# Kernel optimization log

Measured on AMD Instinct MI355X. Metric: run time of the kernel, lower is better.

Reference implementation:

```python
import jax, jax.numpy as jnp
import numpy as np
import math

B, S, D, H = 2, 2048, 1024, 16
HD = D // H  # head_dims = 64


def setup_inputs() -> dict:
    key = jax.random.key(0)
    ks = jax.random.split(key, 8)
    sc = 1.0 / math.sqrt(D)
    return {
        "queries": jax.random.normal(ks[0], (B, S, D), jnp.float32),
        "keys":    jax.random.normal(ks[1], (B, S, D), jnp.float32),
        "values":  jax.random.normal(ks[2], (B, S, D), jnp.float32),
        # causal mask: 1 where attending allowed, 0 where blocked (masked_fill on ==0)
        "mask": jnp.tril(jnp.ones((S, S), jnp.int32)),
        "Wq": jax.random.normal(ks[3], (D, D), jnp.float32) * sc,
        "bq": jnp.zeros((D,), jnp.float32),
        "Wk": jax.random.normal(ks[4], (D, D), jnp.float32) * sc,
        "bk": jnp.zeros((D,), jnp.float32),
        "Wv": jax.random.normal(ks[5], (D, D), jnp.float32) * sc,
        "bv": jnp.zeros((D,), jnp.float32),
        "Wo": jax.random.normal(ks[6], (D, D), jnp.float32) * sc,
        "bo": jnp.zeros((D,), jnp.float32),
    }


def _split_heads(x):
    # (B, S, D) -> (B, H, S, HD)
    return x.reshape(B, S, H, HD).transpose(0, 2, 1, 3)


def reference(queries, keys, values, mask, Wq, bq, Wk, bk, Wv, bv, Wo, bo):
    q = queries @ Wq + bq
    k = keys @ Wk + bk
    # NOTE: faithful to source quirk — V is projected from the ALREADY-PROJECTED keys
    # (original: keys = self.W_keys(keys); values = self.W_values(keys))
    v = k @ Wv + bv
    q, k, v = _split_heads(q), _split_heads(k), _split_heads(v)
    # naive full NxN attention, as in the source
    scores = jnp.einsum("bhqd,bhkd->bhqk", q, k) / math.sqrt(HD)
    scores = jnp.where(mask == 0, jnp.float32(-1e9), scores)
    probs = jax.nn.softmax(scores, axis=-1)
    attn = jnp.einsum("bhqk,bhkd->bhqd", probs, v)
    attn = attn.transpose(0, 2, 1, 3).reshape(B, S, D)
    return attn @ Wo + bo
```

## Files before the change

### kernel.cpp

```cpp
#include <hip/hip_runtime.h>

typedef unsigned short u16;
typedef unsigned int u32;
typedef __bf16 bf16x8 __attribute__((ext_vector_type(8)));
typedef float f32x4 __attribute__((ext_vector_type(4)));
typedef float f32x16 __attribute__((ext_vector_type(16)));
typedef unsigned int u32x4v __attribute__((ext_vector_type(4)));

#define MFMA16(a, b, c) __builtin_amdgcn_mfma_f32_16x16x32_bf16(a, b, c, 0, 0, 0)
#define MFMA32(a, b, c) __builtin_amdgcn_mfma_f32_32x32x16_bf16(a, b, c, 0, 0, 0)

__device__ __forceinline__ void gload16(const void* g, void* l) {
  __builtin_amdgcn_global_load_lds((const __attribute__((address_space(1))) void*)g,
                                   (__attribute__((address_space(3))) void*)l, 16, 0, 0);
}

__device__ __forceinline__ u16 f2bf(float f) {
  u32 u = __builtin_bit_cast(u32, f);
  u += 0x7fffu + ((u >> 16) & 1u);
  return (u16)(u >> 16);
}
__device__ __forceinline__ u32 pack2(float a, float b) {
  u32 r;
  asm("v_cvt_pk_bf16_f32 %0, %1, %2" : "=v"(r) : "v"(a), "v"(b));
  return r;
}

__global__ __launch_bounds__(256) void prep_kernel(
    const float* __restrict__ q, const float* __restrict__ k,
    u16* __restrict__ qb, u16* __restrict__ kb,
    const float* W0, const float* W1, const float* W2, const float* W3,
    u16* T0, u16* T1, u16* T2, u16* T3) {
  __shared__ float tile[64][65];
  const int z = blockIdx.z;
  if (z < 2) {
    const float* src = z ? k : q;
    u16* dst = z ? kb : qb;
    const int bid = blockIdx.y * 16 + blockIdx.x;
    const size_t base = (size_t)bid * 256 + threadIdx.x;
#pragma unroll
    for (int i = 0; i < 16; i++) {
      size_t idx = base + (size_t)i * 65536;
      float4 v = ((const float4*)src)[idx];
      uint2 o;
      o.x = pack2(v.x, v.y);
      o.y = pack2(v.z, v.w);
      ((uint2*)dst)[idx] = o;
    }
    return;
  }
  const float* W = z == 2 ? W0 : z == 3 ? W1 : z == 4 ? W2 : W3;
  u16* T = z == 2 ? T0 : z == 3 ? T1 : z == 4 ? T2 : T3;
  int tr = blockIdx.y * 64, tc = blockIdx.x * 64;
  int tid = threadIdx.x;
  int c4 = (tid & 15) * 4, r0 = tid >> 4;
#pragma unroll
  for (int i = 0; i < 4; i++) {
    int r = r0 + i * 16;
    float4 v = *(const float4*)(W + (size_t)(tr + r) * 1024 + tc + c4);
    tile[r][c4 + 0] = v.x; tile[r][c4 + 1] = v.y;
    tile[r][c4 + 2] = v.z; tile[r][c4 + 3] = v.w;
  }
  __syncthreads();
#pragma unroll
  for (int i = 0; i < 2; i++) {
    int c = tid + i * 256;
    int n = c >> 3, kg = c & 7;
    uint4 o;
    o.x = pack2(tile[kg * 8 + 0][n], tile[kg * 8 + 1][n]);
    o.y = pack2(tile[kg * 8 + 2][n], tile[kg * 8 + 3][n]);
    o.z = pack2(tile[kg * 8 + 4][n], tile[kg * 8 + 5][n]);
    o.w = pack2(tile[kg * 8 + 6][n], tile[kg * 8 + 7][n]);
    *(uint4*)(T + (size_t)(tc + n) * 1024 + tr + kg * 8) = o;
  }
}

template <int MODE>
__global__ __launch_bounds__(256) void gemm_kernel(
    const u16* A0, const u16* B0, const float* bias0, void* C0, float scale0,
    const u16* A1, const u16* B1, const float* bias1, void* C1, float scale1,
    int M, int N, int K) {
  const u16* A = A0; const u16* Bt = B0; const float* bias = bias0; void* Cout = C0;
  float scale = scale0;
  if (blockIdx.z) { A = A1; Bt = B1; bias = bias1; Cout = C1; scale = scale1; }

  __shared__ __attribute__((aligned(16))) char sAB[49152];
  const int tid = threadIdx.x, lane = tid & 63, w = tid >> 6;
  const int l15 = lane & 15, quad = lane >> 4;
  const int wm = (w >> 1) * 64, wn = (w & 1) * 32;
  const int m0 = blockIdx.y * 128, n0 = blockIdx.x * 64;

  const int lrow = lane >> 3, lcg = (lane & 7) ^ lrow;
  const u16* aP[4]; const u16* bP[2];
#pragma unroll
  for (int i = 0; i < 4; i++)
    aP[i] = A + (size_t)(m0 + w * 32 + i * 8 + lrow) * K + lcg * 8;
#pragma unroll
  for (int i = 0; i < 2; i++)
    bP[i] = Bt + (size_t)(n0 + w * 16 + i * 8 + lrow) * K + lcg * 8;

  int aoff[4], boff[2];
#pragma unroll
  for (int t = 0; t < 4; t++) {
    int ra = wm + t * 16 + l15;
    aoff[t] = ra * 128 + ((quad ^ (ra & 7)) * 16);
  }
#pragma unroll
  for (int t = 0; t < 2; t++) {
    int rb = wn + t * 16 + l15;
    boff[t] = 16384 + rb * 128 + ((quad ^ (rb & 7)) * 16);
  }

#pragma unroll
  for (int i = 0; i < 4; i++) { gload16(aP[i], sAB + w * 4096 + i * 1024); aP[i] += 64; }
#pragma unroll
  for (int i = 0; i < 2; i++) { gload16(bP[i], sAB + 16384 + w * 2048 + i * 1024); bP[i] += 64; }

  f32x4 acc[4][2] = {};
  int cur = 0;
  for (int k = 0; k < K; k += 64) {
    __syncthreads();
    if (k + 64 < K) {
      char* dst = sAB + (cur ^ 1) * 24576;
#pragma unroll
      for (int i = 0; i < 4; i++) { gload16(aP[i], dst + w * 4096 + i * 1024); aP[i] += 64; }
#pragma unroll
      for (int i = 0; i < 2; i++) { gload16(bP[i], dst + 16384 + w * 2048 + i * 1024); bP[i] += 64; }
    }
    const char* buf = sAB + cur * 24576;
#pragma unroll
    for (int kt = 0; kt < 2; kt++) {
      bf16x8 af[4], bfr[2];
#pragma unroll
      for (int t = 0; t < 4; t++) af[t] = *(const bf16x8*)(buf + (aoff[t] ^ (kt * 64)));
#pragma unroll
      for (int t = 0; t < 2; t++) bfr[t] = *(const bf16x8*)(buf + (boff[t] ^ (kt * 64)));
#pragma unroll
      for (int mt = 0; mt < 4; mt++)
#pragma unroll
        for (int nt = 0; nt < 2; nt++)
          acc[mt][nt] = MFMA16(af[mt], bfr[nt], acc[mt][nt]);
    }
    cur ^= 1;
  }

#pragma unroll
  for (int nt = 0; nt < 2; nt++) {
    int col = n0 + wn + nt * 16 + l15;
    float bv = bias[col];
#pragma unroll
    for (int mt = 0; mt < 4; mt++) {
      int row = m0 + wm + mt * 16 + quad * 4;
      if (MODE == 0) {
        u16* C = (u16*)Cout;
#pragma unroll
        for (int r = 0; r < 4; r++)
          C[(size_t)(row + r) * N + col] = f2bf((acc[mt][nt][r] + bv) * scale);
      } else if (MODE == 1) {
        u16* C = (u16*)Cout;
        int hh = col >> 6, hd = col & 63;
        int bb = row >> 11, s = row & 2047;
        uint2 o;
        o.x = pack2((acc[mt][nt][0] + bv) * scale, (acc[mt][nt][1] + bv) * scale);
        o.y = pack2((acc[mt][nt][2] + bv) * scale, (acc[mt][nt][3] + bv) * scale);
        *(uint2*)(C + ((size_t)((bb * 16 + hh) * 64 + hd) * 2048 + s)) = o;
      } else {
        float* C = (float*)Cout;
#pragma unroll
        for (int r = 0; r < 4; r++)
          C[(size_t)(row + r) * N + col] = (acc[mt][nt][r] + bv) * scale;
      }
    }
  }
}

__global__ __launch_bounds__(256, 2) void attn_kernel(const u16* __restrict__ qw,
                                                      const u16* __restrict__ kw,
                                                      const u16* __restrict__ vw,
                                                      u16* __restrict__ aout) {
  __shared__ __attribute__((aligned(16))) char sKV[4][16384];
  __shared__ float slq[4][64];
  char* sflat = (char*)sKV;
  const int bh = blockIdx.x, p = blockIdx.y;
  const int b = bh >> 4, h = bh & 15;
  const int tid = threadIdx.x, lane = tid & 63, w = tid >> 6;
  const int g = w & 1, kh = w >> 1;
  const int c = lane & 31, hi = lane >> 5;
  const int lrow = lane >> 3, lcg = (lane & 7) ^ lrow;
  const u16* kb0 = kw + (size_t)(b * 2048) * 1024 + h * 64;
  const u16* vb0 = vw + (size_t)bh * 64 * 2048;

  int koffK[4], koffV[2][2];
  {
    int krow = kh * 32 + c;
#pragma unroll
    for (int kt = 0; kt < 4; kt++)
      koffK[kt] = krow * 128 + (((kt * 2 + hi) ^ (krow & 7)) * 16);
#pragma unroll
    for (int m = 0; m < 2; m++) {
      int vrow = m * 32 + c;
#pragma unroll
      for (int kt2 = 0; kt2 < 2; kt2++)
        koffV[m][kt2] = 8192 + vrow * 128 + ((((kh * 2 + kt2) * 2 + hi) ^ (vrow & 7)) * 16);
    }
  }

  auto stage = [&](int j, int slot) {
    char* dst = sKV[slot];
#pragma unroll
    for (int i = 0; i < 2; i++) {
      int rr = w * 16 + i * 8 + lrow;
      gload16(kb0 + (size_t)(j * 64 + rr) * 1024 + lcg * 8, dst + w * 2048 + i * 1024);
      gload16(vb0 + (size_t)rr * 2048 + j * 64 + lcg * 8, dst + 8192 + w * 2048 + i * 1024);
    }
  };

  for (int phase = 0; phase < 2; ++phase) {
    const int t = phase ? (31 - p) : p;
    __syncthreads();

    bf16x8 qf[2][4];
#pragma unroll
    for (int qb2 = 0; qb2 < 2; qb2++) {
      const u16* qbase =
          qw + (size_t)(b * 2048 + t * 64 + qb2 * 32 + c) * 1024 + h * 64 + hi * 8;
#pragma unroll
      for (int kt = 0; kt < 4; kt++) qf[qb2][kt] = *(const bf16x8*)(qbase + kt * 16);
    }
    stage(0, 0);
    if (t >= 1) stage(1, 1);

    f32x16 o00 = {}, o01 = {}, o10 = {}, o11 = {};
    float ls0 = 0.f, ls1 = 0.f;
    const int R = (t + 2) >> 1;
    for (int r = 0; r < R; ++r) {
      __syncthreads();
      if (2 * r + 2 <= t) stage(2 * r + 2, (2 * r + 2) & 3);
      if (2 * r + 3 <= t) stage(2 * r + 3, (2 * r + 3) & 3);
      const int jg = 2 * r + g;
      if (jg <= t) {
        const char* buf = sKV[jg & 3];
        f32x16 S0 = {}, S1 = {};
        __builtin_amdgcn_s_setprio(1);
#pragma unroll
        for (int kt = 0; kt < 4; kt++) {
          bf16x8 kf = *(const bf16x8*)(buf + koffK[kt]);
          S0 = MFMA32(kf, qf[0][kt], S0);
          S1 = MFMA32(kf, qf[1][kt], S1);
        }
        __builtin_amdgcn_s_setprio(0);
        const bool diag = (jg == t);
        u32 pw0[8], pw1[8];
        auto epack = [&](const f32x16& S, int qc, u32* pw, float& ls) {
          float e[16];
#pragma unroll
          for (int rg = 0; rg < 16; rg++) {
            float ev = __builtin_amdgcn_exp2f(S[rg]);
            if (diag) {
              int row = kh * 32 + (rg & 3) + 8 * (rg >> 2) + 4 * hi;
              if (row > qc) ev = 0.f;
            }
            e[rg] = ev;
          }
          float sAcc = 0.f;
#pragma unroll
          for (int rg = 0; rg < 16; rg += 4)
            sAcc += (e[rg] + e[rg + 1]) + (e[rg + 2] + e[rg + 3]);
          ls += sAcc;
#pragma unroll
          for (int i = 0; i < 8; i++) pw[i] = pack2(e[2 * i], e[2 * i + 1]);
        };
        epack(S0, c, pw0, ls0);
        epack(S1, 32 + c, pw1, ls1);
        __builtin_amdgcn_s_setprio(1);
#pragma unroll
        for (int kt2 = 0; kt2 < 2; kt2++) {
          const int bb = kt2 * 4;
          auto a0 = __builtin_amdgcn_permlane32_swap(pw0[bb + 0], pw0[bb + 2], false, false);
          auto a1 = __builtin_amdgcn_permlane32_swap(pw0[bb + 1], pw0[bb + 3], false, false);
          u32x4v pq0 = {a0[0], a1[0], a0[1], a1[1]};
          bf16x8 pf0 = __builtin_bit_cast(bf16x8, pq0);
          auto b0 = __builtin_amdgcn_permlane32_swap(pw1[bb + 0], pw1[bb + 2], false, false);
          auto b1 = __builtin_amdgcn_permlane32_swap(pw1[bb + 1], pw1[bb + 3], false, false);
          u32x4v pq1 = {b0[0], b1[0], b0[1], b1[1]};
          bf16x8 pf1 = __builtin_bit_cast(bf16x8, pq1);
          bf16x8 v0 = *(const bf16x8*)(buf + koffV[0][kt2]);
          bf16x8 v1 = *(const bf16x8*)(buf + koffV[1][kt2]);
          o00 = MFMA32(v0, pf0, o00);
          o10 = MFMA32(v1, pf0, o10);
          o01 = MFMA32(v0, pf1, o01);
          o11 = MFMA32(v1, pf1, o11);
        }
        __builtin_amdgcn_s_setprio(0);
      }
    }

    ls0 += __shfl_xor(ls0, 32, 64);
    ls1 += __shfl_xor(ls1, 32, 64);
    __syncthreads();
    {
      char* myr = sflat + w * 16384;
      auto putq = [&](int qid, const f32x16& v) {
#pragma unroll
        for (int ch = 0; ch < 4; ch++) {
          f32x4 x = {v[ch * 4 + 0], v[ch * 4 + 1], v[ch * 4 + 2], v[ch * 4 + 3]};
          *(f32x4*)(myr + (qid * 4 + ch) * 1024 + lane * 16) = x;
        }
      };
      putq(0, o00); putq(1, o01); putq(2, o10); putq(3, o11);
      slq[w][hi * 32 + c] = hi ? ls1 : ls0;
    }
    __syncthreads();
    {
      f32x16 acc = {};
#pragma unroll
      for (int wv = 0; wv < 4; wv++)
#pragma unroll
        for (int ch = 0; ch < 4; ch++) {
          f32x4 rr = *(const f32x4*)(sflat + wv * 16384 + (w * 4 + ch) * 1024 + lane * 16);
          acc[ch * 4 + 0] += rr[0]; acc[ch * 4 + 1] += rr[1];
          acc[ch * 4 + 2] += rr[2]; acc[ch * 4 + 3] += rr[3];
        }
      const int q = (w & 1) * 32 + c;
      float lt = ((slq[0][q] + slq[1][q]) + (slq[2][q] + slq[3][q]));
      float inv = 1.0f / lt;
      int token = b * 2048 + t * 64 + q;
      u16* outp = aout + (size_t)token * 1024 + h * 64 + (w >> 1) * 32;
#pragma unroll
      for (int i = 0; i < 4; i++) {
        uint2 ov;
        ov.x = pack2(acc[4 * i + 0] * inv, acc[4 * i + 1] * inv);
        ov.y = pack2(acc[4 * i + 2] * inv, acc[4 * i + 3] * inv);
        *(uint2*)(outp + i * 8 + hi * 4) = ov;
      }
    }
  }
}

extern "C" void kernel_launch(void* const* d_in, const int* in_sizes, int n_in,
                              void* d_out, int out_size, void* d_ws, size_t ws_size,
                              hipStream_t stream) {
  const float* queries = (const float*)d_in[0];
  const float* keys    = (const float*)d_in[1];
  const float* Wq = (const float*)d_in[4];
  const float* bq = (const float*)d_in[5];
  const float* Wk = (const float*)d_in[6];
  const float* bk = (const float*)d_in[7];
  const float* Wv = (const float*)d_in[8];
  const float* bv = (const float*)d_in[9];
  const float* Wo = (const float*)d_in[10];
  const float* bo = (const float*)d_in[11];

  char* ws = (char*)d_ws;
  u16* qb  = (u16*)(ws);
  u16* kb  = (u16*)(ws + (8u << 20));
  u16* qP  = (u16*)(ws + (16u << 20));
  u16* kP  = (u16*)(ws);
  u16* vP  = (u16*)(ws + (8u << 20));
  u16* WqT = (u16*)(ws + (24u << 20));
  u16* WkT = (u16*)(ws + (26u << 20));
  u16* WvT = (u16*)(ws + (28u << 20));
  u16* WoT = (u16*)(ws + (30u << 20));

  const float kscale = 1.4426950408889634f / 8.0f;

  prep_kernel<<<dim3(16, 16, 6), 256, 0, stream>>>(
      queries, keys, qb, kb, Wq, Wk, Wv, Wo, WqT, WkT, WvT, WoT);
  gemm_kernel<0><<<dim3(16, 32, 2), 256, 0, stream>>>(
      qb, WqT, bq, qP, kscale, kb, WkT, bk, kP, 1.0f, 4096, 1024, 1024);
  gemm_kernel<1><<<dim3(16, 32, 1), 256, 0, stream>>>(
      kP, WvT, bv, vP, 1.0f, kP, WvT, bv, vP, 1.0f, 4096, 1024, 1024);
  attn_kernel<<<dim3(32, 16), 256, 0, stream>>>(qP, kP, vP, qP);
  gemm_kernel<2><<<dim3(16, 32, 1), 256, 0, stream>>>(
      qP, WoT, bo, d_out, 1.0f, qP, WoT, bo, d_out, 1.0f, 4096, 1024, 1024);
}
```

Baseline: 213.5 us.

## Run both causal query tiles concurrently in one 512-thread attention block

```diff
diff --git a/kernel.cpp b/kernel.cpp
--- a/kernel.cpp
+++ b/kernel.cpp
@@ -174,7 +174,7 @@
   }
 }
 
-__global__ __launch_bounds__(256, 2) void attn_kernel(const u16* __restrict__ qw,
+__global__ __launch_bounds__(512, 4) void attn_kernel(const u16* __restrict__ qw,
                                                       const u16* __restrict__ kw,
                                                       const u16* __restrict__ vw,
                                                       u16* __restrict__ aout) {
@@ -184,7 +184,10 @@
   const int bh = blockIdx.x, p = blockIdx.y;
   const int b = bh >> 4, h = bh & 15;
   const int tid = threadIdx.x, lane = tid & 63, w = tid >> 6;
-  const int g = w & 1, kh = w >> 1;
+  const int quad = w >> 2, w4 = w & 3;
+  const int g = w & 1, kh = (w >> 1) & 1;
+  const int t = quad ? (31 - p) : p;
+  const int tlong = 31 - p;
   const int c = lane & 31, hi = lane >> 5;
   const int lrow = lane >> 3, lcg = (lane & 7) ^ lrow;
   const u16* kb0 = kw + (size_t)(b * 2048) * 1024 + h * 64;
@@ -207,99 +210,94 @@
 
   auto stage = [&](int j, int slot) {
     char* dst = sKV[slot];
-#pragma unroll
-    for (int i = 0; i < 2; i++) {
-      int rr = w * 16 + i * 8 + lrow;
-      gload16(kb0 + (size_t)(j * 64 + rr) * 1024 + lcg * 8, dst + w * 2048 + i * 1024);
-      gload16(vb0 + (size_t)rr * 2048 + j * 64 + lcg * 8, dst + 8192 + w * 2048 + i * 1024);
-    }
+    int rr = w * 8 + lrow;
+    gload16(kb0 + (size_t)(j * 64 + rr) * 1024 + lcg * 8, dst + w * 1024);
+    gload16(vb0 + (size_t)rr * 2048 + j * 64 + lcg * 8, dst + 8192 + w * 1024);
   };
 
-  for (int phase = 0; phase < 2; ++phase) {
-    const int t = phase ? (31 - p) : p;
+  bf16x8 qf[2][4];
+#pragma unroll
+  for (int qb2 = 0; qb2 < 2; qb2++) {
+    const u16* qbase =
+        qw + (size_t)(b * 2048 + t * 64 + qb2 * 32 + c) * 1024 + h * 64 + hi * 8;
+#pragma unroll
+    for (int kt = 0; kt < 4; kt++) qf[qb2][kt] = *(const bf16x8*)(qbase + kt * 16);
+  }
+  stage(0, 0);
+  stage(1, 1);
+
+  f32x16 o00 = {}, o01 = {}, o10 = {}, o11 = {};
+  float ls0 = 0.f, ls1 = 0.f;
+  const int R = (tlong + 2) >> 1;
+  for (int r = 0; r < R; ++r) {
     __syncthreads();
-
-    bf16x8 qf[2][4];
-#pragma unroll
-    for (int qb2 = 0; qb2 < 2; qb2++) {
-      const u16* qbase =
-          qw + (size_t)(b * 2048 + t * 64 + qb2 * 32 + c) * 1024 + h * 64 + hi * 8;
-#pragma unroll
-      for (int kt = 0; kt < 4; kt++) qf[qb2][kt] = *(const bf16x8*)(qbase + kt * 16);
-    }
-    stage(0, 0);
-    if (t >= 1) stage(1, 1);
-
-    f32x16 o00 = {}, o01 = {}, o10 = {}, o11 = {};
-    float ls0 = 0.f, ls1 = 0.f;
-    const int R = (t + 2) >> 1;
-    for (int r = 0; r < R; ++r) {
-      __syncthreads();
-      if (2 * r + 2 <= t) stage(2 * r + 2, (2 * r + 2) & 3);
-      if (2 * r + 3 <= t) stage(2 * r + 3, (2 * r + 3) & 3);
-      const int jg = 2 * r + g;
-      if (jg <= t) {
-        const char* buf = sKV[jg & 3];
-        f32x16 S0 = {}, S1 = {};
-        __builtin_amdgcn_s_setprio(1);
-#pragma unroll
-        for (int kt = 0; kt < 4; kt++) {
-          bf16x8 kf = *(const bf16x8*)(buf + koffK[kt]);
-          S0 = MFMA32(kf, qf[0][kt], S0);
-          S1 = MFMA32(kf, qf[1][kt], S1);
+    if (2 * r + 2 <= tlong) stage(2 * r + 2, (2 * r + 2) & 3);
+    if (2 * r + 3 <= tlong) stage(2 * r + 3, (2 * r + 3) & 3);
+    const int jg = 2 * r + g;
+    if (jg <= t) {
+      const char* buf = sKV[jg & 3];
+      f32x16 S0 = {}, S1 = {};
+      __builtin_amdgcn_s_setprio(1);
+#pragma unroll
+      for (int kt = 0; kt < 4; kt++) {
+        bf16x8 kf = *(const bf16x8*)(buf + koffK[kt]);
+        S0 = MFMA32(kf, qf[0][kt], S0);
+        S1 = MFMA32(kf, qf[1][kt], S1);
+      }
+      __builtin_amdgcn_s_setprio(0);
+      const bool diag = (jg == t);
+      u32 pw0[8], pw1[8];
+      auto epack = [&](const f32x16& S, int qc, u32* pw, float& ls) {
+        float e[16];
+#pragma unroll
+        for (int rg = 0; rg < 16; rg++) {
+          float ev = __builtin_amdgcn_exp2f(S[rg]);
+          if (diag) {
+            int row = kh * 32 + (rg & 3) + 8 * (rg >> 2) + 4 * hi;
+            if (row > qc) ev = 0.f;
+          }
+          e[rg] = ev;
         }
-        __builtin_amdgcn_s_setprio(0);
-        const bool diag = (jg == t);
-        u32 pw0[8], pw1[8];
-        auto epack = [&](const f32x16& S, int qc, u32* pw, float& ls) {
-          float e[16];
-#pragma unroll
-          for (int rg = 0; rg < 16; rg++) {
-            float ev = __builtin_amdgcn_exp2f(S[rg]);
-            if (diag) {
-              int row = kh * 32 + (rg & 3) + 8 * (rg >> 2) + 4 * hi;
-              if (row > qc) ev = 0.f;
-            }
-            e[rg] = ev;
-          }
-          float sAcc = 0.f;
-#pragma unroll
-          for (int rg = 0; rg < 16; rg += 4)
-            sAcc += (e[rg] + e[rg + 1]) + (e[rg + 2] + e[rg + 3]);
-          ls += sAcc;
-#pragma unroll
-          for (int i = 0; i < 8; i++) pw[i] = pack2(e[2 * i], e[2 * i + 1]);
-        };
-        epack(S0, c, pw0, ls0);
-        epack(S1, 32 + c, pw1, ls1);
-        __builtin_amdgcn_s_setprio(1);
-#pragma unroll
-        for (int kt2 = 0; kt2 < 2; kt2++) {
-          const int bb = kt2 * 4;
-          auto a0 = __builtin_amdgcn_permlane32_swap(pw0[bb + 0], pw0[bb + 2], false, false);
-          auto a1 = __builtin_amdgcn_permlane32_swap(pw0[bb + 1], pw0[bb + 3], false, false);
-          u32x4v pq0 = {a0[0], a1[0], a0[1], a1[1]};
-          bf16x8 pf0 = __builtin_bit_cast(bf16x8, pq0);
-          auto b0 = __builtin_amdgcn_permlane32_swap(pw1[bb + 0], pw1[bb + 2], false, false);
-          auto b1 = __builtin_amdgcn_permlane32_swap(pw1[bb + 1], pw1[bb + 3], false, false);
-          u32x4v pq1 = {b0[0], b1[0], b0[1], b1[1]};
-          bf16x8 pf1 = __builtin_bit_cast(bf16x8, pq1);
-          bf16x8 v0 = *(const bf16x8*)(buf + koffV[0][kt2]);
-          bf16x8 v1 = *(const bf16x8*)(buf + koffV[1][kt2]);
-          o00 = MFMA32(v0, pf0, o00);
-          o10 = MFMA32(v1, pf0, o10);
-          o01 = MFMA32(v0, pf1, o01);
-          o11 = MFMA32(v1, pf1, o11);
-        }
-        __builtin_amdgcn_s_setprio(0);
+        float sAcc = 0.f;
+#pragma unroll
+        for (int rg = 0; rg < 16; rg += 4)
+          sAcc += (e[rg] + e[rg + 1]) + (e[rg + 2] + e[rg + 3]);
+        ls += sAcc;
+#pragma unroll
+        for (int i = 0; i < 8; i++) pw[i] = pack2(e[2 * i], e[2 * i + 1]);
+      };
+      epack(S0, c, pw0, ls0);
+      epack(S1, 32 + c, pw1, ls1);
+      __builtin_amdgcn_s_setprio(1);
+#pragma unroll
+      for (int kt2 = 0; kt2 < 2; kt2++) {
+        const int bb = kt2 * 4;
+        auto a0 = __builtin_amdgcn_permlane32_swap(pw0[bb + 0], pw0[bb + 2], false, false);
+        auto a1 = __builtin_amdgcn_permlane32_swap(pw0[bb + 1], pw0[bb + 3], false, false);
+        u32x4v pq0 = {a0[0], a1[0], a0[1], a1[1]};
+        bf16x8 pf0 = __builtin_bit_cast(bf16x8, pq0);
+        auto b0 = __builtin_amdgcn_permlane32_swap(pw1[bb + 0], pw1[bb + 2], false, false);
+        auto b1 = __builtin_amdgcn_permlane32_swap(pw1[bb + 1], pw1[bb + 3], false, false);
+        u32x4v pq1 = {b0[0], b1[0], b0[1], b1[1]};
+        bf16x8 pf1 = __builtin_bit_cast(bf16x8, pq1);
+        bf16x8 v0 = *(const bf16x8*)(buf + koffV[0][kt2]);
+        bf16x8 v1 = *(const bf16x8*)(buf + koffV[1][kt2]);
+        o00 = MFMA32(v0, pf0, o00);
+        o10 = MFMA32(v1, pf0, o10);
+        o01 = MFMA32(v0, pf1, o01);
+        o11 = MFMA32(v1, pf1, o11);
       }
-    }
-
-    ls0 += __shfl_xor(ls0, 32, 64);
-    ls1 += __shfl_xor(ls1, 32, 64);
+      __builtin_amdgcn_s_setprio(0);
+    }
+  }
+
+  ls0 += __shfl_xor(ls0, 32, 64);
+  ls1 += __shfl_xor(ls1, 32, 64);
+#pragma unroll
+  for (int qd = 0; qd < 2; ++qd) {
     __syncthreads();
-    {
-      char* myr = sflat + w * 16384;
+    if (quad == qd) {
+      char* myr = sflat + w4 * 16384;
       auto putq = [&](int qid, const f32x16& v) {
 #pragma unroll
         for (int ch = 0; ch < 4; ch++) {
@@ -308,24 +306,24 @@
         }
       };
       putq(0, o00); putq(1, o01); putq(2, o10); putq(3, o11);
-      slq[w][hi * 32 + c] = hi ? ls1 : ls0;
+      slq[w4][hi * 32 + c] = hi ? ls1 : ls0;
     }
     __syncthreads();
-    {
+    if (quad == qd) {
       f32x16 acc = {};
 #pragma unroll
       for (int wv = 0; wv < 4; wv++)
 #pragma unroll
         for (int ch = 0; ch < 4; ch++) {
-          f32x4 rr = *(const f32x4*)(sflat + wv * 16384 + (w * 4 + ch) * 1024 + lane * 16);
+          f32x4 rr = *(const f32x4*)(sflat + wv * 16384 + (w4 * 4 + ch) * 1024 + lane * 16);
           acc[ch * 4 + 0] += rr[0]; acc[ch * 4 + 1] += rr[1];
           acc[ch * 4 + 2] += rr[2]; acc[ch * 4 + 3] += rr[3];
         }
-      const int q = (w & 1) * 32 + c;
+      const int q = (w4 & 1) * 32 + c;
       float lt = ((slq[0][q] + slq[1][q]) + (slq[2][q] + slq[3][q]));
       float inv = 1.0f / lt;
       int token = b * 2048 + t * 64 + q;
-      u16* outp = aout + (size_t)token * 1024 + h * 64 + (w >> 1) * 32;
+      u16* outp = aout + (size_t)token * 1024 + h * 64 + (w4 >> 1) * 32;
 #pragma unroll
       for (int i = 0; i < 4; i++) {
         uint2 ov;
@@ -370,7 +368,7 @@
       qb, WqT, bq, qP, kscale, kb, WkT, bk, kP, 1.0f, 4096, 1024, 1024);
   gemm_kernel<1><<<dim3(16, 32, 1), 256, 0, stream>>>(
       kP, WvT, bv, vP, 1.0f, kP, WvT, bv, vP, 1.0f, 4096, 1024, 1024);
-  attn_kernel<<<dim3(32, 16), 256, 0, stream>>>(qP, kP, vP, qP);
+  attn_kernel<<<dim3(32, 16), 512, 0, stream>>>(qP, kP, vP, qP);
   gemm_kernel<2><<<dim3(16, 32, 1), 256, 0, stream>>>(
       qP, WoT, bo, d_out, 1.0f, qP, WoT, bo, d_out, 1.0f, 4096, 1024, 1024);
 }
```

Result: slower. 244.1 us (+14.3%).
